# Kernel optimization log

Measured on AMD Instinct MI355X. Metric: run time of the kernel, lower is better.

## Reference

```python
import jax, jax.numpy as jnp
import numpy as np

N_GENE, N_CPG, N_MIRNA = 20000, 60000, 2000
HID, H, NL = 128, 8, 2
C = HID // H
B = 64
NEG_SLOPE = 0.2
LN_EPS = 1e-5
# edge types in HeteroConv order: (src_node_idx, dst_node_idx); node order: 0=gene,1=cpg,2=mirna
EDGE_META = [(1, 0), (0, 1), (2, 0), (0, 2), (0, 0), (0, 0), (1, 1), (2, 2)]


def layernorm(x, g, b):
    mu = jnp.mean(x, axis=-1, keepdims=True)
    var = jnp.mean(jnp.square(x - mu), axis=-1, keepdims=True)
    return (x - mu) * jax.lax.rsqrt(var + LN_EPS) * g + b


def gatv2_conv(x_src, x_dst, ei, Wl, Wr, att, bias):
    """PyG GATv2Conv, add_self_loops=False, concat heads, eval mode (no dropout)."""
    src, dst = ei[0], ei[1]
    n_dst = x_dst.shape[0]
    hs = (x_src @ Wl).reshape(-1, H, C)   # lin_l -> source features [Ns,H,C]
    hd = (x_dst @ Wr).reshape(-1, H, C)   # lin_r -> target features [Nd,H,C]
    e = jax.nn.leaky_relu(hs[src] + hd[dst], NEG_SLOPE)   # [E,H,C]
    logits = jnp.einsum('ehc,hc->eh', e, att)             # [E,H]
    # segment softmax over destination nodes
    m = jax.ops.segment_max(logits, dst, num_segments=n_dst)
    a = jnp.exp(logits - m[dst])
    s = jax.ops.segment_sum(a, dst, num_segments=n_dst)
    alpha = a / (s[dst] + 1e-16)                          # [E,H]
    msg = (hs[src] * alpha[:, :, None]).reshape(-1, HID)  # [E,HID]
    out = jax.ops.segment_sum(msg, dst, num_segments=n_dst)
    return out + bias


def setup_inputs() -> dict:
    key = jax.random.key(0)
    ks = list(jax.random.split(key, 40))
    nk = lambda: ks.pop()
    rn = lambda shape, s=0.05: jax.random.normal(nk(), shape, jnp.float32) * s

    def edges(E, Ns, Nd):
        src = jax.random.randint(nk(), (E,), 0, Ns, jnp.int32)
        dst = jax.random.randint(nk(), (E,), 0, Nd, jnp.int32)
        return jnp.stack([src, dst])

    def self_loops(N):
        ar = jnp.arange(N, dtype=jnp.int32)
        return jnp.stack([ar, ar])

    inp = {
        'batch_gene': rn((B, N_GENE), 1.0),
        'batch_meth': rn((B, N_CPG), 1.0),
        'batch_mirna': rn((B, N_MIRNA), 1.0),
        'emb_gene': rn((N_GENE, HID)),
        'emb_cpg': rn((N_CPG, HID)),
        'emb_mirna': rn((N_MIRNA, HID)),
        'Wl': rn((NL, 8, HID, HID)),
        'Wr': rn((NL, 8, HID, HID)),
        'att': rn((NL, 8, H, C)),
        'bias': rn((NL, 8, HID), 0.01),
        'ln_gamma': jnp.ones((NL, 3, HID), jnp.float32),
        'ln_beta': jnp.zeros((NL, 3, HID), jnp.float32),
        'out_gamma': jnp.ones((3, HID), jnp.float32),
        'out_beta': jnp.zeros((3, HID), jnp.float32),
        'ei_cg': edges(500000, N_CPG, N_GENE),
        'ei_gc': edges(500000, N_GENE, N_CPG),
        'ei_mg': edges(150000, N_MIRNA, N_GENE),
        'ei_gm': edges(150000, N_GENE, N_MIRNA),
        'ei_gg': edges(500000, N_GENE, N_GENE),
        'ei_sg': self_loops(N_GENE),
        'ei_sc': self_loops(N_CPG),
        'ei_sm': self_loops(N_MIRNA),
    }
    return inp


def forward(batch_gene, batch_meth, batch_mirna, emb_gene, emb_cpg, emb_mirna,
            Wl, Wr, att, bias, ln_gamma, ln_beta, out_gamma, out_beta, edge_list):
    x = [emb_gene, emb_cpg, emb_mirna]  # 0=gene,1=cpg,2=mirna
    for l in range(NL):
        agg = [jnp.zeros_like(x[0]), jnp.zeros_like(x[1]), jnp.zeros_like(x[2])]
        for t, (ei, (si, di)) in enumerate(zip(edge_list, EDGE_META)):
            agg[di] = agg[di] + gatv2_conv(x[si], x[di], ei,
                                           Wl[l, t], Wr[l, t], att[l, t], bias[l, t])
        # ELU + residual + LayerNorm per node type (dropout=0 / eval)
        x = [layernorm(x[i] + jax.nn.elu(agg[i]), ln_gamma[l, i], ln_beta[l, i])
             for i in range(3)]
    z_gene = layernorm(batch_gene @ x[0] / np.sqrt(N_GENE), out_gamma[0], out_beta[0])
    z_cpg = layernorm(batch_meth @ x[1] / np.sqrt(N_CPG), out_gamma[1], out_beta[1])
    z_mirna = layernorm(batch_mirna @ x[2] / np.sqrt(N_MIRNA), out_gamma[2], out_beta[2])
    return (z_gene, z_cpg, z_mirna)


def reference(batch_gene, batch_meth, batch_mirna, emb_gene, emb_cpg, emb_mirna,
              Wl, Wr, att, bias, ln_gamma, ln_beta, out_gamma, out_beta,
              ei_cg, ei_gc, ei_mg, ei_gm, ei_gg, ei_sg, ei_sc, ei_sm):
    edge_list = [ei_cg, ei_gc, ei_mg, ei_gm, ei_gg, ei_sg, ei_sc, ei_sm]
    return forward(batch_gene, batch_meth, batch_mirna, emb_gene, emb_cpg, emb_mirna,
                   Wl, Wr, att, bias, ln_gamma, ln_beta, out_gamma, out_beta, edge_list)
```

## Files before the change

### kernel.cpp

```cpp
#include <hip/hip_runtime.h>
#include <math.h>

typedef __attribute__((ext_vector_type(4))) float f32x4;
typedef __attribute__((ext_vector_type(2))) float f32x2;
typedef __attribute__((ext_vector_type(8))) short bf16x8;

__device__ __forceinline__ float b2f(unsigned short u) {
  return __uint_as_float(((unsigned)u) << 16);
}
__device__ __forceinline__ unsigned short f2b(float f) {
  unsigned x = __float_as_uint(f);
  unsigned r = (x + 0x7FFFu + ((x >> 16) & 1u)) >> 16;
  return (unsigned short)r;
}
__device__ __forceinline__ f32x2 bf2x2(unsigned u) {
  f32x2 r;
  r.x = __uint_as_float(u << 16);
  r.y = __uint_as_float(u & 0xFFFF0000u);
  return r;
}
__device__ __forceinline__ f32x2 pk_max(f32x2 a, f32x2 b) {
#if __has_builtin(__builtin_elementwise_max)
  return __builtin_elementwise_max(a, b);
#else
  f32x2 r; r.x = fmaxf(a.x, b.x); r.y = fmaxf(a.y, b.y); return r;
#endif
}
__device__ __forceinline__ f32x2 pk_fma(f32x2 a, f32x2 b, f32x2 c) {
#if __has_builtin(__builtin_elementwise_fma)
  return __builtin_elementwise_fma(a, b, c);
#else
  f32x2 r; r.x = fmaf(a.x, b.x, c.x); r.y = fmaf(a.y, b.y, c.y); return r;
#endif
}

#if __has_builtin(__builtin_amdgcn_cvt_pk_f32_fp8)
template<bool HI>
__device__ __forceinline__ f32x2 fp8x2_dec(unsigned w) {
  return __builtin_amdgcn_cvt_pk_f32_fp8(w, HI);
}
#else
__device__ __forceinline__ float fp8_dec1(unsigned b) {
  unsigned s = b >> 7, e = (b >> 3) & 15, m = b & 7;
  float v = (e == 0) ? (float)m * 0.001953125f
                     : __uint_as_float(((e - 7 + 127) << 23) | (m << 20));
  return s ? -v : v;
}
template<bool HI>
__device__ __forceinline__ f32x2 fp8x2_dec(unsigned w) {
  unsigned h = HI ? (w >> 16) : w;
  f32x2 r; r.x = fp8_dec1(h & 0xFF); r.y = fp8_dec1((h >> 8) & 0xFF);
  return r;
}
#endif
#if __has_builtin(__builtin_amdgcn_cvt_pk_fp8_f32)
template<bool HI>
__device__ __forceinline__ int fp8x2_enc(float a, float b, int old) {
  return __builtin_amdgcn_cvt_pk_fp8_f32(a, b, old, HI);
}
#else
__device__ __forceinline__ unsigned fp8_enc1(float f) {
  unsigned s = (__float_as_uint(f) >> 31) << 7;
  float a = fabsf(f);
  if (a >= 448.f) return s | 0x7E;
  if (a < 0.015625f) {
    int m = (int)(a * 512.f + 0.5f);
    return s | (unsigned)(m > 7 ? 7 : m);
  }
  int ex; (void)frexpf(a, &ex);
  int E = ex - 1;
  float sig = a * exp2f((float)(-E));
  int m = (int)((sig - 1.f) * 8.f + 0.5f);
  if (m == 8) { m = 0; E += 1; }
  if (E > 8) return s | 0x7E;
  return s | (unsigned)((E + 7) << 3) | (unsigned)m;
}
template<bool HI>
__device__ __forceinline__ int fp8x2_enc(float a, float b, int old) {
  unsigned pk = fp8_enc1(a) | (fp8_enc1(b) << 8);
  return HI ? ((old & 0x0000FFFF) | (int)(pk << 16))
            : ((old & (int)0xFFFF0000) | (int)pk);
}
#endif

__global__ __launch_bounds__(256) void prep_w(
    const float* __restrict__ Wl, const float* __restrict__ Wr,
    unsigned short* __restrict__ wt)
{
  int elem = blockIdx.x * 256 + threadIdx.x;
  int mat = elem >> 14;
  int c = (elem >> 7) & 127;
  int k = elem & 127;
  const float* srcb = (mat & 1) ? Wr : Wl;
  wt[elem] = f2b(srcb[((long)(mat >> 1) << 14) + (k << 7) + c]);
}

__global__ __launch_bounds__(256) void cast_all(
    const float* __restrict__ e0, const float* __restrict__ e1,
    const float* __restrict__ e2, unsigned short* __restrict__ x0,
    unsigned short* __restrict__ x1, unsigned short* __restrict__ x2,
    int n0, int n1, int n2)
{
  int i = blockIdx.x * 256 + threadIdx.x;
  const float* s; unsigned short* d; int loc = i;
  if (loc < n0) { s = e0; d = x0; }
  else {
    loc -= n0;
    if (loc < n1) { s = e1; d = x1; }
    else { loc -= n1; if (loc >= n2) return; s = e2; d = x2; }
  }
  float4 v = *(const float4*)(s + (long)loc * 4);
  ushort4 o = {f2b(v.x), f2b(v.y), f2b(v.z), f2b(v.w)};
  *(ushort4*)(d + (long)loc * 4) = o;
}

__global__ __launch_bounds__(256) void cast_fp8(
    const unsigned short* __restrict__ src, unsigned char* __restrict__ dst,
    long n8)
{
  long i = (long)blockIdx.x * 256 + threadIdx.x;
  if (i >= n8) return;
  uint4 v = *(const uint4*)(src + i * 8);
  f32x2 a = bf2x2(v.x), b = bf2x2(v.y), c = bf2x2(v.z), d = bf2x2(v.w);
  int lo = 0, hi = 0;
  lo = fp8x2_enc<false>(a.x, a.y, lo);
  lo = fp8x2_enc<true>(b.x, b.y, lo);
  hi = fp8x2_enc<false>(c.x, c.y, hi);
  hi = fp8x2_enc<true>(d.x, d.y, hi);
  uint2 o = {(unsigned)lo, (unsigned)hi};
  *(uint2*)(dst + i * 8) = o;
}

__device__ __forceinline__ void mproj_tile(
    char* lx, char* lw, const unsigned short* __restrict__ xb,
    const unsigned short* __restrict__ wt, void* __restrict__ outv,
    int N, long r0, int tid, int mode)
{
#pragma unroll
  for (int i = 0; i < 8; ++i) {
    int ch = i * 256 + tid;
    int row = ch >> 4, k0 = (ch & 15) << 3;
    uint4 xv = {0u, 0u, 0u, 0u};
    if (r0 + row < N) xv = *(const uint4*)(xb + (r0 + row) * 128 + k0);
    *(uint4*)(lx + ((row * 256 + k0 * 2) ^ ((row & 7) << 4))) = xv;
    uint4 wv = *(const uint4*)(wt + (long)ch * 8);
    *(uint4*)(lw + ((ch * 16) ^ ((row & 7) << 4))) = wv;
  }
  __syncthreads();

  const int lane = tid & 63;
  const int lr = lane & 15, lk = lane >> 4;
  const int rbase = (tid >> 6) * 32;
  f32x4 acc[2][8] = {};
#pragma unroll
  for (int kb = 0; kb < 4; ++kb) {
    int k = kb * 32 + lk * 8;
    int ra = rbase + lr;
    bf16x8 a0 = *(const bf16x8*)(lx + ((ra * 256 + k * 2) ^ ((ra & 7) << 4)));
    int rb = rbase + 16 + lr;
    bf16x8 a1 = *(const bf16x8*)(lx + ((rb * 256 + k * 2) ^ ((rb & 7) << 4)));
#pragma unroll
    for (int cc = 0; cc < 8; ++cc) {
      int col = cc * 16 + lr;
      bf16x8 bfr = *(const bf16x8*)(lw + ((col * 256 + k * 2) ^ ((col & 7) << 4)));
      acc[0][cc] = __builtin_amdgcn_mfma_f32_16x16x32_bf16(a0, bfr, acc[0][cc], 0, 0, 0);
      acc[1][cc] = __builtin_amdgcn_mfma_f32_16x16x32_bf16(a1, bfr, acc[1][cc], 0, 0, 0);
    }
  }
  __syncthreads();
#pragma unroll
  for (int rt = 0; rt < 2; ++rt) {
    int rowb = rbase + rt * 16 + lk * 4;
#pragma unroll
    for (int cc = 0; cc < 8; ++cc) {
      int col = cc * 16 + lr;
#pragma unroll
      for (int q = 0; q < 4; ++q) {
        long row = r0 + rowb + q;
        if (row < N) {
          if (mode == 2)
            ((unsigned short*)outv)[row * 128 + col] = f2b(acc[rt][cc][q]);
          else
            ((float*)outv)[row * 128 + col] = acc[rt][cc][q];
        }
      }
    }
  }
}

struct PJob { const unsigned short* x; const unsigned short* wt; void* out; int N; int mode; };
struct PArgs { PJob j[13]; int off[14]; };

__global__ __launch_bounds__(256) void mproj_all(PArgs a)
{
  __shared__ __align__(16) char lx[32768];
  __shared__ __align__(16) char lw[32768];
  int blk = blockIdx.x, t = 0;
  while (blk >= a.off[t + 1]) ++t;
  const PJob& J = a.j[t];
  mproj_tile(lx, lw, J.x, J.wt, J.out, J.N, (long)(blk - a.off[t]) * 128,
             threadIdx.x, J.mode);
}

struct BArgs {
  const int* src[5]; const int* dst[5];
  int* cnt[5];
  int* tmp[5];
  int* rs[5];
  int* csrc[5];
  int E[5], Nd[5], NB[5], B[5];
  int cOff[6], fOff[6];
};

__global__ __launch_bounds__(256) void bucket_count(BArgs a)
{
  __shared__ int h[512];
  int blk = blockIdx.x, t = 0;
  while (blk >= a.cOff[t + 1]) ++t;
  int lb = blk - a.cOff[t];
  int B = a.B[t], NB = a.NB[t], E = a.E[t];
  for (int i = threadIdx.x; i < B; i += 256) h[i] = 0;
  __syncthreads();
  const int* dst = a.dst[t];
  int base = lb * 4096;
#pragma unroll
  for (int j = 0; j < 16; ++j) {
    int e = base + j * 256 + threadIdx.x;
    if (e < E) atomicAdd(&h[dst[e] >> 7], 1);
  }
  __syncthreads();
  int* cnt = a.cnt[t];
  for (int b = threadIdx.x; b < B; b += 256) cnt[b * NB + lb] = h[b];
}

__global__ __launch_bounds__(1024) void bucket_scan(BArgs a)
{
  int t = blockIdx.x;
  int n = a.B[t] * a.NB[t];
  int* dp = a.cnt[t];
  __shared__ int wsum[16];
  __shared__ int sbase, ctot;
  int tid = threadIdx.x;
  int lane = tid & 63, wid = tid >> 6;
  if (tid == 0) sbase = 0;
  __syncthreads();
  for (int chunk = 0; chunk < n; chunk += 16384) {
    int idx0 = chunk + tid * 16;
    int v[16], lsum = 0;
#pragma unroll
    for (int j = 0; j < 16; ++j) {
      v[j] = (idx0 + j < n) ? dp[idx0 + j] : 0;
      lsum += v[j];
    }
    int sc = lsum;
#pragma unroll
    for (int o = 1; o < 64; o <<= 1) {
      int u = __shfl_up(sc, o);
      if (lane >= o) sc += u;
    }
    if (lane == 63) wsum[wid] = sc;
    __syncthreads();
    if (wid == 0) {
      int w = (lane < 16) ? wsum[lane] : 0;
      int s2 = w;
#pragma unroll
      for (int o = 1; o < 16; o <<= 1) {
        int u = __shfl_up(s2, o);
        if (lane >= o) s2 += u;
      }
      if (lane < 16) wsum[lane] = s2 - w;
      if (lane == 15) ctot = s2;
    }
    __syncthreads();
    int excl = sbase + wsum[wid] + (sc - lsum);
#pragma unroll
    for (int j = 0; j < 16; ++j) {
      if (idx0 + j < n) dp[idx0 + j] = excl;
      excl += v[j];
    }
    __syncthreads();
    if (tid == 0) sbase += ctot;
    __syncthreads();
  }
}

__global__ __launch_bounds__(256) void bucket_scatter(BArgs a)
{
  __shared__ int cur[512];
  int blk = blockIdx.x, t = 0;
  while (blk >= a.cOff[t + 1]) ++t;
  int lb = blk - a.cOff[t];
  int B = a.B[t], NB = a.NB[t], E = a.E[t];
  const int* cnt = a.cnt[t];
  for (int b = threadIdx.x; b < B; b += 256) cur[b] = cnt[b * NB + lb];
  __syncthreads();
  const int* src = a.src[t];
  const int* dst = a.dst[t];
  int* tmp = a.tmp[t];
  int base = lb * 4096;
#pragma unroll
  for (int j = 0; j < 16; ++j) {
    int e = base + j * 256 + threadIdx.x;
    if (e < E) {
      int dv = dst[e];
      int pos = atomicAdd(&cur[dv >> 7], 1);
      tmp[pos] = ((dv & 127) << 16) | src[e];
    }
  }
}

__global__ __launch_bounds__(256) void bucket_finalize(BArgs a)
{
  __shared__ int h[128], sc[128], ex[128], cur[128];
  int blk = blockIdx.x, t = 0;
  while (blk >= a.fOff[t + 1]) ++t;
  int b = blk - a.fOff[t];
  int B = a.B[t], NB = a.NB[t], E = a.E[t], Nd = a.Nd[t];
  const int* cnt = a.cnt[t];
  const int* tmp = a.tmp[t];
  int* rs = a.rs[t];
  int* csrc = a.csrc[t];
  int tid = threadIdx.x;
  int beg = cnt[b * NB];
  int end = (b + 1 < B) ? cnt[(b + 1) * NB] : E;
  if (tid < 128) h[tid] = 0;
  __syncthreads();
  for (int i = beg + tid; i < end; i += 256)
    atomicAdd(&h[tmp[i] >> 16], 1);
  __syncthreads();
  if (tid < 128) sc[tid] = h[tid];
  __syncthreads();
#pragma unroll
  for (int off = 1; off < 128; off <<= 1) {
    int v = (tid < 128 && tid >= off) ? sc[tid - off] : 0;
    __syncthreads();
    if (tid < 128) sc[tid] += v;
    __syncthreads();
  }
  if (tid < 128) {
    ex[tid] = sc[tid] - h[tid];
    cur[tid] = 0;
    int dg = b * 128 + tid;
    if (dg < Nd) rs[dg] = beg + ex[tid];
  }
  if (b == B - 1 && tid == 0) rs[Nd] = E;
  __syncthreads();
  for (int i = beg + tid; i < end; i += 256) {
    int v = tmp[i];
    int d = v >> 16;
    int r = atomicAdd(&cur[d], 1);
    csrc[beg + ex[d] + r] = v & 0xFFFF;
  }
}

struct GSeg {
  const int* rs[3]; const int* csrc[3];
  const unsigned char* hs[3]; const unsigned short* hd[3];
  const float* att[3];
  float* agg; int Nd; int ntypes;
};
struct GArgs { GSeg s[3]; int off[4]; };

__global__ __launch_bounds__(256) void gat_gather_all(GArgs g)
{
  int blk = blockIdx.x, si = 0;
  while (blk >= g.off[si + 1]) ++si;
  const GSeg& sg = g.s[si];
  int d = (blk - g.off[si]) * 4 + (threadIdx.x >> 6);
  if (d >= sg.Nd) return;
  int lane = threadIdx.x & 63;
  int q = lane >> 4, j = lane & 15;
  f32x2 T0 = {0.f, 0.f}, T1 = {0.f, 0.f}, T2 = {0.f, 0.f}, T3 = {0.f, 0.f};
  for (int k = 0; k < sg.ntypes; ++k) {
    const float* ap = sg.att[k] + 8 * j;
    float4 aa = *(const float4*)ap;
    float4 ab = *(const float4*)(ap + 4);
    f32x2 A0 = {aa.x, aa.y}, A1 = {aa.z, aa.w};
    f32x2 A2 = {ab.x, ab.y}, A3 = {ab.z, ab.w};
    uint4 hu = *((const uint4*)(sg.hd[k] + (long)d * 128) + j);
    f32x2 H0 = bf2x2(hu.x), H1 = bf2x2(hu.y);
    f32x2 H2 = bf2x2(hu.z), H3 = bf2x2(hu.w);
    const int* cs = sg.csrc[k];
    const unsigned char* hsk = sg.hs[k];
    int beg = sg.rs[k][d], end = sg.rs[k][d + 1];
    f32x2 n0 = {0.f, 0.f}, n1 = {0.f, 0.f}, n2 = {0.f, 0.f}, n3 = {0.f, 0.f};
    float D = 0.f;

#define GA_EDGE(U)                                                          \
    {                                                                       \
      f32x2 h0 = fp8x2_dec<false>((U).x), h1 = fp8x2_dec<true>((U).x);      \
      f32x2 h2 = fp8x2_dec<false>((U).y), h3 = fp8x2_dec<true>((U).y);      \
      f32x2 v0 = h0 + H0, v1 = h1 + H1, v2 = h2 + H2, v3 = h3 + H3;         \
      v0 = pk_max(v0, v0 * 0.2f);                                           \
      v1 = pk_max(v1, v1 * 0.2f);                                           \
      v2 = pk_max(v2, v2 * 0.2f);                                           \
      v3 = pk_max(v3, v3 * 0.2f);                                           \
      f32x2 pv = pk_fma(v0, A0, pk_fma(v1, A1, pk_fma(v2, A2, v3 * A3)));   \
      float p = pv.x + pv.y;                                                \
      p += __shfl_xor(p, 1);                                                \
      float a = __expf(fminf(p, 60.f));                                     \
      f32x2 av = {a, a};                                                    \
      n0 = pk_fma(h0, av, n0);                                              \
      n1 = pk_fma(h1, av, n1);                                              \
      n2 = pk_fma(h2, av, n2);                                              \
      n3 = pk_fma(h3, av, n3);                                              \
      D += a;                                                               \
    }

    int i = beg + q;
    for (; i + 4 < end; i += 8) {
      int s0 = cs[i], s1 = cs[i + 4];
      uint2 u0 = *((const uint2*)(hsk + (long)s0 * 128) + j);
      uint2 u1 = *((const uint2*)(hsk + (long)s1 * 128) + j);
      GA_EDGE(u0);
      GA_EDGE(u1);
    }
    if (i < end) {
      int s = cs[i];
      uint2 u = *((const uint2*)(hsk + (long)s * 128) + j);
      GA_EDGE(u);
    }
#undef GA_EDGE

#pragma unroll
    for (int o = 16; o < 64; o <<= 1) {
      n0.x += __shfl_xor(n0.x, o); n0.y += __shfl_xor(n0.y, o);
      n1.x += __shfl_xor(n1.x, o); n1.y += __shfl_xor(n1.y, o);
      n2.x += __shfl_xor(n2.x, o); n2.y += __shfl_xor(n2.y, o);
      n3.x += __shfl_xor(n3.x, o); n3.y += __shfl_xor(n3.y, o);
      D += __shfl_xor(D, o);
    }
    float inv = 1.f / (D + 1e-16f);
    f32x2 iv = {inv, inv};
    T0 = pk_fma(n0, iv, T0);
    T1 = pk_fma(n1, iv, T1);
    T2 = pk_fma(n2, iv, T2);
    T3 = pk_fma(n3, iv, T3);
  }
  if (q == 0) {
    float* apg = sg.agg + (long)d * 128 + 8 * j;
    float4 c0 = *(const float4*)apg;
    float4 c1 = *(const float4*)(apg + 4);
    c0.x += T0.x; c0.y += T0.y; c0.z += T1.x; c0.w += T1.y;
    c1.x += T2.x; c1.y += T2.y; c1.z += T3.x; c1.w += T3.y;
    *(float4*)apg = c0;
    *(float4*)(apg + 4) = c1;
  }
}

struct LJob {
  const float* xin; float* xf; unsigned short* xb;
  const float* agg; const float* biasl; int tmask;
  const float* gam; const float* bet; int N;
};
struct LArgs { LJob j[3]; int off[4]; };

__global__ __launch_bounds__(256) void update_ln_all(LArgs a)
{
  int blk = blockIdx.x, t = 0;
  while (blk >= a.off[t + 1]) ++t;
  const LJob& J = a.j[t];
  int row = (blk - a.off[t]) * 4 + (threadIdx.x >> 6);
  int lane = threadIdx.x & 63;
  if (row >= J.N) return;
  float bs0 = 0.f, bs1 = 0.f;
#pragma unroll
  for (int tt = 0; tt < 8; ++tt)
    if (J.tmask & (1 << tt)) {
      bs0 += J.biasl[tt * 128 + lane];
      bs1 += J.biasl[tt * 128 + 64 + lane];
    }
  long base = (long)row * 128;
  float v0 = J.agg[base + lane] + bs0, v1 = J.agg[base + 64 + lane] + bs1;
  v0 = v0 > 0.f ? v0 : __expf(v0) - 1.f;
  v1 = v1 > 0.f ? v1 : __expf(v1) - 1.f;
  float x0 = J.xin[base + lane] + v0, x1 = J.xin[base + 64 + lane] + v1;
  float s = x0 + x1;
#pragma unroll
  for (int o = 32; o > 0; o >>= 1) s += __shfl_xor(s, o);
  float mu = s * 0.0078125f;
  float dd0 = x0 - mu, dd1 = x1 - mu;
  float q = dd0 * dd0 + dd1 * dd1;
#pragma unroll
  for (int o = 32; o > 0; o >>= 1) q += __shfl_xor(q, o);
  float r = rsqrtf(q * 0.0078125f + 1e-5f);
  float y0 = dd0 * r * J.gam[lane] + J.bet[lane];
  float y1 = dd1 * r * J.gam[64 + lane] + J.bet[64 + lane];
  J.xf[base + lane] = y0; J.xf[base + 64 + lane] = y1;
  J.xb[base + lane] = f2b(y0); J.xb[base + 64 + lane] = f2b(y1);
}

struct ZArgs {
  const float* batch[3]; const float* x[3]; float* zp[3]; int N[3];
  int off[4];
};

__global__ __launch_bounds__(256) void zgemm_all(ZArgs z)
{
  __shared__ __align__(16) float xl[64 * 128];
  __shared__ __align__(16) float bl[64 * 65];
  int blk = blockIdx.x, s = 0;
  while (blk >= z.off[s + 1]) ++s;
  int chunk = blk - z.off[s];
  const float* batch = z.batch[s];
  const float* x = z.x[s];
  int N = z.N[s];
  int tid = threadIdx.x;
  int n0 = chunk * 64;
  for (int i = tid; i < 64 * 128; i += 256) {
    int nn = i >> 7;
    xl[i] = (n0 + nn < N) ? x[(long)(n0 + nn) * 128 + (i & 127)] : 0.f;
  }
  for (int i = tid; i < 64 * 64; i += 256) {
    int b = i >> 6, nn = i & 63;
    bl[nn * 65 + b] = (n0 + nn < N) ? batch[(long)b * N + n0 + nn] : 0.f;
  }
  __syncthreads();
  int cg = (tid & 31) * 4;
  int bg = (tid >> 5) * 8;
  float acc[8][4] = {};
  for (int nn = 0; nn < 64; ++nn) {
    float4 xv = *(const float4*)(xl + nn * 128 + cg);
#pragma unroll
    for (int i = 0; i < 8; ++i) {
      float bv = bl[nn * 65 + bg + i];
      acc[i][0] = fmaf(bv, xv.x, acc[i][0]);
      acc[i][1] = fmaf(bv, xv.y, acc[i][1]);
      acc[i][2] = fmaf(bv, xv.z, acc[i][2]);
      acc[i][3] = fmaf(bv, xv.w, acc[i][3]);
    }
  }
  float* zp = z.zp[s] + (long)chunk * 8192;
#pragma unroll
  for (int i = 0; i < 8; ++i) {
    float4 v = {acc[i][0], acc[i][1], acc[i][2], acc[i][3]};
    *(float4*)(zp + (bg + i) * 128 + cg) = v;
  }
}

__global__ __launch_bounds__(256) void zreduce(
    const float* __restrict__ zp0, const float* __restrict__ zp1,
    const float* __restrict__ zp2, int G0, int G1, int G2,
    float s0, float s1, float s2, float* __restrict__ zpre)
{
  int blk = blockIdx.x;
  int ty = blk >> 5;
  int i = (blk & 31) * 256 + threadIdx.x;
  const float* zp = ty == 0 ? zp0 : (ty == 1 ? zp1 : zp2);
  int G = ty == 0 ? G0 : (ty == 1 ? G1 : G2);
  float sc = ty == 0 ? s0 : (ty == 1 ? s1 : s2);
  float a[16];
#pragma unroll
  for (int u = 0; u < 16; ++u) a[u] = 0.f;
  int g = 0;
  for (; g + 16 <= G; g += 16) {
#pragma unroll
    for (int u = 0; u < 16; ++u) a[u] += zp[(long)(g + u) * 8192 + i];
  }
  for (; g < G; ++g) a[0] += zp[(long)g * 8192 + i];
  float s = (((a[0] + a[1]) + (a[2] + a[3])) + ((a[4] + a[5]) + (a[6] + a[7])))
          + (((a[8] + a[9]) + (a[10] + a[11])) + ((a[12] + a[13]) + (a[14] + a[15])));
  zpre[ty * 8192 + i] = s * sc;
}

__global__ __launch_bounds__(256) void final_ln(
    const float* __restrict__ zpre, const float* __restrict__ gam,
    const float* __restrict__ bet, float* __restrict__ out)
{
  int row = blockIdx.x * 4 + (threadIdx.x >> 6);
  int lane = threadIdx.x & 63;
  if (row >= 192) return;
  int ty = row >> 6;
  long base = (long)row * 128;
  float x0 = zpre[base + lane], x1 = zpre[base + 64 + lane];
  float s = x0 + x1;
#pragma unroll
  for (int o = 32; o > 0; o >>= 1) s += __shfl_xor(s, o);
  float mu = s * 0.0078125f;
  float d0 = x0 - mu, d1 = x1 - mu;
  float q = d0 * d0 + d1 * d1;
#pragma unroll
  for (int o = 32; o > 0; o >>= 1) q += __shfl_xor(q, o);
  float r = rsqrtf(q * 0.0078125f + 1e-5f);
  out[base + lane]      = d0 * r * gam[ty * 128 + lane]      + bet[ty * 128 + lane];
  out[base + 64 + lane] = d1 * r * gam[ty * 128 + 64 + lane] + bet[ty * 128 + 64 + lane];
}

extern "C" void kernel_launch(void* const* d_in, const int* in_sizes, int n_in,
                              void* d_out, int out_size, void* d_ws, size_t ws_size,
                              hipStream_t stream)
{
  const float* batchp[3] = {(const float*)d_in[0], (const float*)d_in[1],
                            (const float*)d_in[2]};
  const float* emb[3] = {(const float*)d_in[3], (const float*)d_in[4],
                         (const float*)d_in[5]};
  const float* Wl   = (const float*)d_in[6];
  const float* Wr   = (const float*)d_in[7];
  const float* att  = (const float*)d_in[8];
  const float* bias = (const float*)d_in[9];
  const float* lng  = (const float*)d_in[10];
  const float* lnb  = (const float*)d_in[11];
  const float* outg = (const float*)d_in[12];
  const float* outb = (const float*)d_in[13];
  const int* eiP[8]; int E[8];
  for (int t = 0; t < 8; ++t) { eiP[t] = (const int*)d_in[14 + t]; E[t] = in_sizes[14 + t] / 2; }
  int Nn[3] = {in_sizes[3] / 128, in_sizes[4] / 128, in_sizes[5] / 128};
  long Ntot = (long)Nn[0] + Nn[1] + Nn[2];

  const int SI[5] = {1, 0, 2, 0, 0};
  const int DI[5] = {0, 1, 0, 2, 0};
  const int TMASK[3] = {0x35, 0x42, 0x88};

  char* p = (char*)d_ws;
  auto carve = [&](size_t b) -> void* {
    void* r = (void*)p; p += (b + 255) & ~(size_t)255; return r;
  };
  float* xf[3];
  for (int ty = 0; ty < 3; ++ty) xf[ty] = (float*)carve((size_t)Nn[ty] * 128 * 4);
  unsigned short* xb[3];
  for (int ty = 0; ty < 3; ++ty) xb[ty] = (unsigned short*)carve((size_t)Nn[ty] * 128 * 2);
  float* aggAll = (float*)carve((size_t)Ntot * 128 * 4);
  float* agg[3] = {aggAll, aggAll + (long)Nn[0] * 128, aggAll + ((long)Nn[0] + Nn[1]) * 128};
  unsigned short* hsT[5];
  unsigned short* hdT[5];
  char* projRegion = p;
  for (int t = 0; t < 5; ++t) hsT[t] = (unsigned short*)carve((size_t)Nn[SI[t]] * 128 * 2);
  for (int t = 0; t < 5; ++t) hdT[t] = (unsigned short*)carve((size_t)Nn[DI[t]] * 128 * 2);
  size_t projBytes = (size_t)(p - projRegion);
  long hsElems = 0;
  for (int t = 0; t < 5; ++t) hsElems += (long)Nn[SI[t]] * 128;
  unsigned char* hs8base = (unsigned char*)carve((size_t)hsElems);
  unsigned char* hs8T[5];
  {
    unsigned char* q8 = hs8base;
    for (int t = 0; t < 5; ++t) { hs8T[t] = q8; q8 += (long)Nn[SI[t]] * 128; }
  }
  float* zpre = (float*)carve(3 * 64 * 128 * 4);
  unsigned short* wtb = (unsigned short*)carve((size_t)32 * 16384 * 2);

  BArgs ba;
  {
    int cOff = 0, fOff = 0;
    for (int t = 0; t < 5; ++t) {
      int nd = Nn[DI[t]];
      ba.src[t] = eiP[t];
      ba.dst[t] = eiP[t] + E[t];
      ba.E[t] = E[t];
      ba.Nd[t] = nd;
      ba.NB[t] = (E[t] + 4095) / 4096;
      ba.B[t] = (nd + 127) / 128;
      ba.cnt[t] = (int*)carve((size_t)ba.B[t] * ba.NB[t] * 4);
      ba.tmp[t] = (int*)carve((size_t)E[t] * 4);
      ba.rs[t] = (int*)carve((size_t)(nd + 1) * 4);
      ba.csrc[t] = (int*)carve((size_t)E[t] * 4);
      ba.cOff[t] = cOff; cOff += ba.NB[t];
      ba.fOff[t] = fOff; fOff += ba.B[t];
    }
    ba.cOff[5] = cOff;
    ba.fOff[5] = fOff;
  }
  if ((size_t)(p - (char*)d_ws) > ws_size) return;

  int nch[3];
  for (int ty = 0; ty < 3; ++ty) nch[ty] = (Nn[ty] + 63) / 64;
  float* zp[3];
  zp[0] = (float*)projRegion;
  zp[1] = zp[0] + (long)nch[0] * 8192;
  zp[2] = zp[1] + (long)nch[1] * 8192;
  if ((size_t)(nch[0] + nch[1] + nch[2]) * 8192 * 4 > projBytes) return;

  auto WTB = [&](int l, int t, int which) {
    return wtb + ((long)((l * 8 + t) * 2 + which) << 14);
  };

  prep_w<<<2048, 256, 0, stream>>>(Wl, Wr, wtb);
  {
    int n0 = Nn[0] * 32, n1 = Nn[1] * 32, n2 = Nn[2] * 32;
    cast_all<<<(int)((n0 + n1 + n2 + 255) / 256), 256, 0, stream>>>(
        emb[0], emb[1], emb[2], xb[0], xb[1], xb[2], n0, n1, n2);
  }

  bucket_count<<<ba.cOff[5], 256, 0, stream>>>(ba);
  bucket_scan<<<5, 1024, 0, stream>>>(ba);
  bucket_scatter<<<ba.cOff[5], 256, 0, stream>>>(ba);
  bucket_finalize<<<ba.fOff[5], 256, 0, stream>>>(ba);

  const int GT[3][3] = {{0, 2, 4}, {1, -1, -1}, {3, -1, -1}};
  const int GN[3] = {3, 1, 1};

  for (int l = 0; l < 2; ++l) {
    const float* xinf[3] = {l == 0 ? emb[0] : xf[0],
                            l == 0 ? emb[1] : xf[1],
                            l == 0 ? emb[2] : xf[2]};
    PArgs pa;
    {
      int off = 0, j = 0;
      auto add = [&](const unsigned short* x, const unsigned short* wt,
                     void* out, int N, int mode) {
        pa.j[j] = {x, wt, out, N, mode};
        pa.off[j] = off;
        off += (N + 127) / 128;
        ++j;
      };
      for (int t = 0; t < 5; ++t) add(xb[SI[t]], WTB(l, t, 0), hsT[t], Nn[SI[t]], 2);
      for (int t = 0; t < 5; ++t) add(xb[DI[t]], WTB(l, t, 1), hdT[t], Nn[DI[t]], 2);
      for (int ty = 0; ty < 3; ++ty) add(xb[ty], WTB(l, 5 + ty, 0), agg[ty], Nn[ty], 0);
      pa.off[13] = off;
      mproj_all<<<off, 256, 0, stream>>>(pa);
    }
    {
      long n8 = hsElems / 8;
      cast_fp8<<<(int)((n8 + 255) / 256), 256, 0, stream>>>(hsT[0], hs8base, n8);
    }
    GArgs ga;
    {
      int off = 0;
      for (int s = 0; s < 3; ++s) {
        GSeg& sg = ga.s[s];
        sg.agg = agg[s];
        sg.Nd = Nn[s];
        sg.ntypes = GN[s];
        for (int k = 0; k < GN[s]; ++k) {
          int t = GT[s][k];
          sg.rs[k] = ba.rs[t];
          sg.csrc[k] = ba.csrc[t];
          sg.hs[k] = hs8T[t];
          sg.hd[k] = hdT[t];
          sg.att[k] = att + (long)(l * 8 + t) * 128;
        }
        ga.off[s] = off;
        off += (Nn[s] + 3) / 4;
      }
      ga.off[3] = off;
      gat_gather_all<<<off, 256, 0, stream>>>(ga);
    }
    LArgs la;
    {
      int off = 0;
      for (int ty = 0; ty < 3; ++ty) {
        la.j[ty] = {xinf[ty], xf[ty], xb[ty], agg[ty],
                    bias + (long)l * 8 * 128, TMASK[ty],
                    lng + (long)(l * 3 + ty) * 128,
                    lnb + (long)(l * 3 + ty) * 128, Nn[ty]};
        la.off[ty] = off;
        off += (Nn[ty] + 3) / 4;
      }
      la.off[3] = off;
      update_ln_all<<<off, 256, 0, stream>>>(la);
    }
  }

  ZArgs za;
  {
    int off = 0;
    for (int ty = 0; ty < 3; ++ty) {
      za.batch[ty] = batchp[ty];
      za.x[ty] = xf[ty];
      za.zp[ty] = zp[ty];
      za.N[ty] = Nn[ty];
      za.off[ty] = off;
      off += nch[ty];
    }
    za.off[3] = off;
    zgemm_all<<<off, 256, 0, stream>>>(za);
  }
  zreduce<<<96, 256, 0, stream>>>(
      zp[0], zp[1], zp[2], nch[0], nch[1], nch[2],
      (float)(1.0 / sqrt((double)Nn[0])), (float)(1.0 / sqrt((double)Nn[1])),
      (float)(1.0 / sqrt((double)Nn[2])), zpre);
  final_ln<<<48, 256, 0, stream>>>(zpre, outg, outb, (float*)d_out);
}
```

Before: 578.3 us.

## Fuse bias/ELU/residual/LayerNorm into GAT gather and merge final z reduction with LN

The separate update_ln_all kernel is folded into the gather epilogue. The gather now adds self-loop aggregation, a precomputed bias sum and ELU, then applies residual LayerNorm across 16 lanes and writes fp32 and bf16 node features directly. This removes the agg write/read round trip and one launch per layer. Source indices in the gather loop are now prefetched one iteration ahead, and zreduce and final_ln are merged into one zfinal kernel. The trade-off is higher register pressure in the gather kernel, and the final z reduction runs with half as many blocks.

```diff
diff --git a/kernel.cpp b/kernel.cpp
--- a/kernel.cpp
+++ b/kernel.cpp
@@ -112,6 +112,20 @@
   float4 v = *(const float4*)(s + (long)loc * 4);
   ushort4 o = {f2b(v.x), f2b(v.y), f2b(v.z), f2b(v.w)};
   *(ushort4*)(d + (long)loc * 4) = o;
+}
+
+__global__ __launch_bounds__(128) void prep_bias(
+    const float* __restrict__ bias, float* __restrict__ bsum)
+{
+  int c = threadIdx.x;
+  const int TM[3] = {0x35, 0x42, 0x88};
+  for (int l = 0; l < 2; ++l)
+    for (int ty = 0; ty < 3; ++ty) {
+      float s = 0.f;
+      for (int t = 0; t < 8; ++t)
+        if (TM[ty] & (1 << t)) s += bias[(l * 8 + t) * 128 + c];
+      bsum[(l * 3 + ty) * 128 + c] = s;
+    }
 }
 
 __global__ __launch_bounds__(256) void cast_fp8(
@@ -357,11 +371,16 @@
   const int* rs[3]; const int* csrc[3];
   const unsigned char* hs[3]; const unsigned short* hd[3];
   const float* att[3];
-  float* agg; int Nd; int ntypes;
+  const float* aggSelf;
+  const float* xin;
+  float* xf; unsigned short* xb;
+  const float* bsum;
+  const float* gam; const float* bet;
+  int Nd; int ntypes;
 };
 struct GArgs { GSeg s[3]; int off[4]; };
 
-__global__ __launch_bounds__(256) void gat_gather_all(GArgs g)
+__global__ __launch_bounds__(256) void gat_gather_ln(GArgs g)
 {
   int blk = blockIdx.x, si = 0;
   while (blk >= g.off[si + 1]) ++si;
@@ -408,16 +427,18 @@
     }
 
     int i = beg + q;
+    int sA = (i < end) ? cs[i] : 0;
+    int sB = (i + 4 < end) ? cs[i + 4] : 0;
     for (; i + 4 < end; i += 8) {
-      int s0 = cs[i], s1 = cs[i + 4];
-      uint2 u0 = *((const uint2*)(hsk + (long)s0 * 128) + j);
-      uint2 u1 = *((const uint2*)(hsk + (long)s1 * 128) + j);
+      uint2 u0 = *((const uint2*)(hsk + (long)sA * 128) + j);
+      uint2 u1 = *((const uint2*)(hsk + (long)sB * 128) + j);
+      sA = (i + 8 < end) ? cs[i + 8] : 0;
+      sB = (i + 12 < end) ? cs[i + 12] : 0;
       GA_EDGE(u0);
       GA_EDGE(u1);
     }
     if (i < end) {
-      int s = cs[i];
-      uint2 u = *((const uint2*)(hsk + (long)s * 128) + j);
+      uint2 u = *((const uint2*)(hsk + (long)sA * 128) + j);
       GA_EDGE(u);
     }
 #undef GA_EDGE
@@ -437,57 +458,59 @@
     T2 = pk_fma(n2, iv, T2);
     T3 = pk_fma(n3, iv, T3);
   }
+
+  long base = (long)d * 128 + 8 * j;
+  float4 sA0 = *(const float4*)(sg.aggSelf + base);
+  float4 sA1 = *(const float4*)(sg.aggSelf + base + 4);
+  float4 bb0 = *(const float4*)(sg.bsum + 8 * j);
+  float4 bb1 = *(const float4*)(sg.bsum + 8 * j + 4);
+  float v[8];
+  v[0] = sA0.x + T0.x + bb0.x; v[1] = sA0.y + T0.y + bb0.y;
+  v[2] = sA0.z + T1.x + bb0.z; v[3] = sA0.w + T1.y + bb0.w;
+  v[4] = sA1.x + T2.x + bb1.x; v[5] = sA1.y + T2.y + bb1.y;
+  v[6] = sA1.z + T3.x + bb1.z; v[7] = sA1.w + T3.y + bb1.w;
+#pragma unroll
+  for (int c = 0; c < 8; ++c) v[c] = v[c] > 0.f ? v[c] : __expf(v[c]) - 1.f;
+  float4 xi0 = *(const float4*)(sg.xin + base);
+  float4 xi1 = *(const float4*)(sg.xin + base + 4);
+  float xr[8] = {xi0.x + v[0], xi0.y + v[1], xi0.z + v[2], xi0.w + v[3],
+                 xi1.x + v[4], xi1.y + v[5], xi1.z + v[6], xi1.w + v[7]};
+  float ssum = ((xr[0] + xr[1]) + (xr[2] + xr[3])) +
+               ((xr[4] + xr[5]) + (xr[6] + xr[7]));
+#pragma unroll
+  for (int o = 1; o < 16; o <<= 1) ssum += __shfl_xor(ssum, o);
+  float mu = ssum * 0.0078125f;
+  float qs = 0.f;
+#pragma unroll
+  for (int c = 0; c < 8; ++c) { float dd = xr[c] - mu; qs += dd * dd; }
+#pragma unroll
+  for (int o = 1; o < 16; o <<= 1) qs += __shfl_xor(qs, o);
+  float rr = rsqrtf(qs * 0.0078125f + 1e-5f);
+  float4 g0 = *(const float4*)(sg.gam + 8 * j);
+  float4 g1 = *(const float4*)(sg.gam + 8 * j + 4);
+  float4 e0 = *(const float4*)(sg.bet + 8 * j);
+  float4 e1 = *(const float4*)(sg.bet + 8 * j + 4);
+  float y[8];
+  y[0] = (xr[0] - mu) * rr * g0.x + e0.x;
+  y[1] = (xr[1] - mu) * rr * g0.y + e0.y;
+  y[2] = (xr[2] - mu) * rr * g0.z + e0.z;
+  y[3] = (xr[3] - mu) * rr * g0.w + e0.w;
+  y[4] = (xr[4] - mu) * rr * g1.x + e1.x;
+  y[5] = (xr[5] - mu) * rr * g1.y + e1.y;
+  y[6] = (xr[6] - mu) * rr * g1.z + e1.z;
+  y[7] = (xr[7] - mu) * rr * g1.w + e1.w;
   if (q == 0) {
-    float* apg = sg.agg + (long)d * 128 + 8 * j;
-    float4 c0 = *(const float4*)apg;
-    float4 c1 = *(const float4*)(apg + 4);
-    c0.x += T0.x; c0.y += T0.y; c0.z += T1.x; c0.w += T1.y;
-    c1.x += T2.x; c1.y += T2.y; c1.z += T3.x; c1.w += T3.y;
-    *(float4*)apg = c0;
-    *(float4*)(apg + 4) = c1;
-  }
-}
-
-struct LJob {
-  const float* xin; float* xf; unsigned short* xb;
-  const float* agg; const float* biasl; int tmask;
-  const float* gam; const float* bet; int N;
-};
-struct LArgs { LJob j[3]; int off[4]; };
-
-__global__ __launch_bounds__(256) void update_ln_all(LArgs a)
-{
-  int blk = blockIdx.x, t = 0;
-  while (blk >= a.off[t + 1]) ++t;
-  const LJob& J = a.j[t];
-  int row = (blk - a.off[t]) * 4 + (threadIdx.x >> 6);
-  int lane = threadIdx.x & 63;
-  if (row >= J.N) return;
-  float bs0 = 0.f, bs1 = 0.f;
-#pragma unroll
-  for (int tt = 0; tt < 8; ++tt)
-    if (J.tmask & (1 << tt)) {
-      bs0 += J.biasl[tt * 128 + lane];
-      bs1 += J.biasl[tt * 128 + 64 + lane];
-    }
-  long base = (long)row * 128;
-  float v0 = J.agg[base + lane] + bs0, v1 = J.agg[base + 64 + lane] + bs1;
-  v0 = v0 > 0.f ? v0 : __expf(v0) - 1.f;
-  v1 = v1 > 0.f ? v1 : __expf(v1) - 1.f;
-  float x0 = J.xin[base + lane] + v0, x1 = J.xin[base + 64 + lane] + v1;
-  float s = x0 + x1;
-#pragma unroll
-  for (int o = 32; o > 0; o >>= 1) s += __shfl_xor(s, o);
-  float mu = s * 0.0078125f;
-  float dd0 = x0 - mu, dd1 = x1 - mu;
-  float q = dd0 * dd0 + dd1 * dd1;
-#pragma unroll
-  for (int o = 32; o > 0; o >>= 1) q += __shfl_xor(q, o);
-  float r = rsqrtf(q * 0.0078125f + 1e-5f);
-  float y0 = dd0 * r * J.gam[lane] + J.bet[lane];
-  float y1 = dd1 * r * J.gam[64 + lane] + J.bet[64 + lane];
-  J.xf[base + lane] = y0; J.xf[base + 64 + lane] = y1;
-  J.xb[base + lane] = f2b(y0); J.xb[base + 64 + lane] = f2b(y1);
+    float4 o0 = {y[0], y[1], y[2], y[3]};
+    float4 o1 = {y[4], y[5], y[6], y[7]};
+    *(float4*)(sg.xf + base) = o0;
+    *(float4*)(sg.xf + base + 4) = o1;
+    uint4 ub;
+    ub.x = (unsigned)f2b(y[0]) | ((unsigned)f2b(y[1]) << 16);
+    ub.y = (unsigned)f2b(y[2]) | ((unsigned)f2b(y[3]) << 16);
+    ub.z = (unsigned)f2b(y[4]) | ((unsigned)f2b(y[5]) << 16);
+    ub.w = (unsigned)f2b(y[6]) | ((unsigned)f2b(y[7]) << 16);
+    *(uint4*)(sg.xb + base) = ub;
+  }
 }
 
 struct ZArgs {
@@ -538,50 +561,44 @@
   }
 }
 
-__global__ __launch_bounds__(256) void zreduce(
+__global__ __launch_bounds__(256) void zfinal(
     const float* __restrict__ zp0, const float* __restrict__ zp1,
     const float* __restrict__ zp2, int G0, int G1, int G2,
-    float s0, float s1, float s2, float* __restrict__ zpre)
+    float s0, float s1, float s2, const float* __restrict__ gam,
+    const float* __restrict__ bet, float* __restrict__ out)
 {
   int blk = blockIdx.x;
-  int ty = blk >> 5;
-  int i = (blk & 31) * 256 + threadIdx.x;
+  int ty = blk >> 4;
+  int rowL = (blk & 15) * 4 + (threadIdx.x >> 6);
+  int lane = threadIdx.x & 63;
   const float* zp = ty == 0 ? zp0 : (ty == 1 ? zp1 : zp2);
   int G = ty == 0 ? G0 : (ty == 1 ? G1 : G2);
   float sc = ty == 0 ? s0 : (ty == 1 ? s1 : s2);
-  float a[16];
-#pragma unroll
-  for (int u = 0; u < 16; ++u) a[u] = 0.f;
+  long i0 = rowL * 128 + lane, i1 = i0 + 64;
+  float a0[8], a1[8];
+#pragma unroll
+  for (int u = 0; u < 8; ++u) { a0[u] = 0.f; a1[u] = 0.f; }
   int g = 0;
-  for (; g + 16 <= G; g += 16) {
-#pragma unroll
-    for (int u = 0; u < 16; ++u) a[u] += zp[(long)(g + u) * 8192 + i];
-  }
-  for (; g < G; ++g) a[0] += zp[(long)g * 8192 + i];
-  float s = (((a[0] + a[1]) + (a[2] + a[3])) + ((a[4] + a[5]) + (a[6] + a[7])))
-          + (((a[8] + a[9]) + (a[10] + a[11])) + ((a[12] + a[13]) + (a[14] + a[15])));
-  zpre[ty * 8192 + i] = s * sc;
-}
-
-__global__ __launch_bounds__(256) void final_ln(
-    const float* __restrict__ zpre, const float* __restrict__ gam,
-    const float* __restrict__ bet, float* __restrict__ out)
-{
-  int row = blockIdx.x * 4 + (threadIdx.x >> 6);
-  int lane = threadIdx.x & 63;
-  if (row >= 192) return;
-  int ty = row >> 6;
-  long base = (long)row * 128;
-  float x0 = zpre[base + lane], x1 = zpre[base + 64 + lane];
+  for (; g + 8 <= G; g += 8) {
+#pragma unroll
+    for (int u = 0; u < 8; ++u) {
+      a0[u] += zp[(long)(g + u) * 8192 + i0];
+      a1[u] += zp[(long)(g + u) * 8192 + i1];
+    }
+  }
+  for (; g < G; ++g) { a0[0] += zp[(long)g * 8192 + i0]; a1[0] += zp[(long)g * 8192 + i1]; }
+  float x0 = (((a0[0] + a0[1]) + (a0[2] + a0[3])) + ((a0[4] + a0[5]) + (a0[6] + a0[7]))) * sc;
+  float x1 = (((a1[0] + a1[1]) + (a1[2] + a1[3])) + ((a1[4] + a1[5]) + (a1[6] + a1[7]))) * sc;
   float s = x0 + x1;
 #pragma unroll
   for (int o = 32; o > 0; o >>= 1) s += __shfl_xor(s, o);
   float mu = s * 0.0078125f;
   float d0 = x0 - mu, d1 = x1 - mu;
-  float q = d0 * d0 + d1 * d1;
-#pragma unroll
-  for (int o = 32; o > 0; o >>= 1) q += __shfl_xor(q, o);
-  float r = rsqrtf(q * 0.0078125f + 1e-5f);
+  float qv = d0 * d0 + d1 * d1;
+#pragma unroll
+  for (int o = 32; o > 0; o >>= 1) qv += __shfl_xor(qv, o);
+  float r = rsqrtf(qv * 0.0078125f + 1e-5f);
+  long base = (long)(ty * 64 + rowL) * 128;
   out[base + lane]      = d0 * r * gam[ty * 128 + lane]      + bet[ty * 128 + lane];
   out[base + 64 + lane] = d1 * r * gam[ty * 128 + 64 + lane] + bet[ty * 128 + 64 + lane];
 }
@@ -609,7 +626,6 @@
 
   const int SI[5] = {1, 0, 2, 0, 0};
   const int DI[5] = {0, 1, 0, 2, 0};
-  const int TMASK[3] = {0x35, 0x42, 0x88};
 
   char* p = (char*)d_ws;
   auto carve = [&](size_t b) -> void* {
@@ -635,7 +651,7 @@
     unsigned char* q8 = hs8base;
     for (int t = 0; t < 5; ++t) { hs8T[t] = q8; q8 += (long)Nn[SI[t]] * 128; }
   }
-  float* zpre = (float*)carve(3 * 64 * 128 * 4);
+  float* bsumBuf = (float*)carve(2 * 3 * 128 * 4);
   unsigned short* wtb = (unsigned short*)carve((size_t)32 * 16384 * 2);
 
   BArgs ba;
@@ -679,6 +695,7 @@
     cast_all<<<(int)((n0 + n1 + n2 + 255) / 256), 256, 0, stream>>>(
         emb[0], emb[1], emb[2], xb[0], xb[1], xb[2], n0, n1, n2);
   }
+  prep_bias<<<1, 128, 0, stream>>>(bias, bsumBuf);
 
   bucket_count<<<ba.cOff[5], 256, 0, stream>>>(ba);
   bucket_scan<<<5, 1024, 0, stream>>>(ba);
@@ -717,7 +734,13 @@
       int off = 0;
       for (int s = 0; s < 3; ++s) {
         GSeg& sg = ga.s[s];
-        sg.agg = agg[s];
+        sg.aggSelf = agg[s];
+        sg.xin = xinf[s];
+        sg.xf = xf[s];
+        sg.xb = xb[s];
+        sg.bsum = bsumBuf + (long)(l * 3 + s) * 128;
+        sg.gam = lng + (long)(l * 3 + s) * 128;
+        sg.bet = lnb + (long)(l * 3 + s) * 128;
         sg.Nd = Nn[s];
         sg.ntypes = GN[s];
         for (int k = 0; k < GN[s]; ++k) {
@@ -732,21 +755,7 @@
         off += (Nn[s] + 3) / 4;
       }
       ga.off[3] = off;
-      gat_gather_all<<<off, 256, 0, stream>>>(ga);
-    }
-    LArgs la;
-    {
-      int off = 0;
-      for (int ty = 0; ty < 3; ++ty) {
-        la.j[ty] = {xinf[ty], xf[ty], xb[ty], agg[ty],
-                    bias + (long)l * 8 * 128, TMASK[ty],
-                    lng + (long)(l * 3 + ty) * 128,
-                    lnb + (long)(l * 3 + ty) * 128, Nn[ty]};
-        la.off[ty] = off;
-        off += (Nn[ty] + 3) / 4;
-      }
-      la.off[3] = off;
-      update_ln_all<<<off, 256, 0, stream>>>(la);
+      gat_gather_ln<<<off, 256, 0, stream>>>(ga);
     }
   }
 
@@ -764,9 +773,8 @@
     za.off[3] = off;
     zgemm_all<<<off, 256, 0, stream>>>(za);
   }
-  zreduce<<<96, 256, 0, stream>>>(
+  zfinal<<<48, 256, 0, stream>>>(
       zp[0], zp[1], zp[2], nch[0], nch[1], nch[2],
       (float)(1.0 / sqrt((double)Nn[0])), (float)(1.0 / sqrt((double)Nn[1])),
-      (float)(1.0 / sqrt((double)Nn[2])), zpre);
-  final_ln<<<48, 256, 0, stream>>>(zpre, outg, outb, (float*)d_out);
-}
+      (float)(1.0 / sqrt((double)Nn[2])), outg, outb, (float*)d_out);
+}
```

Measured after the change: 558.5 us. 3.4% less time.
